# Optimization experiments

Hardware: AMD Instinct MI355X
Metric: run time of the kernel (lower is better)

## Reference

```python
import jax, jax.numpy as jnp
import numpy as np

B, L, D, H = 4, 2048, 2048, 16
HD = D // H
ROPE_BASE = 10000.0


def _rope_cos_sin(seq_len, dim):
    # torchtune-style: theta_i = base^{-2i/dim}, angles[t, i] = t * theta_i
    inv_freq = 1.0 / (ROPE_BASE ** (jnp.arange(0, dim, 2, dtype=jnp.float32) / dim))  # [dim/2]
    angles = jnp.arange(seq_len, dtype=jnp.float32)[:, None] * inv_freq[None, :]  # [L, dim/2]
    return jnp.cos(angles), jnp.sin(angles)


def _apply_rope(x, cos, sin):
    # x: [B, L, H, hd]; rotate interleaved pairs (x0, x1)
    x1 = x[..., 0::2]  # [B, L, H, hd/2]
    x2 = x[..., 1::2]
    c = cos[None, :, None, :]
    s = sin[None, :, None, :]
    o1 = x1 * c - x2 * s
    o2 = x2 * c + x1 * s
    return jnp.stack([o1, o2], axis=-1).reshape(x.shape)


def setup_inputs() -> dict:
    key = jax.random.key(0)
    k1, k2, k3 = jax.random.split(key, 3)
    x = jax.random.normal(k1, (B, L, D), dtype=jnp.float32)
    w_qkv = jax.random.normal(k2, (3 * D, D), dtype=jnp.float32) * (D ** -0.5)
    w_o = jax.random.normal(k3, (D, D), dtype=jnp.float32) * (D ** -0.5)
    return {"x": x, "w_qkv": w_qkv, "w_o": w_o}


def reference(x, w_qkv, w_o):
    qkv = jnp.einsum("bld,ed->ble", x, w_qkv)  # [B, L, 3D]
    q, k, v = jnp.split(qkv, 3, axis=-1)
    q = q.reshape(B, L, H, HD)
    k = k.reshape(B, L, H, HD)
    v = v.reshape(B, L, H, HD)
    cos, sin = _rope_cos_sin(L, HD)
    q = _apply_rope(q, cos, sin)
    k = _apply_rope(k, cos, sin)
    # [B, H, L, hd]
    q = q.transpose(0, 2, 1, 3)
    k = k.transpose(0, 2, 1, 3)
    v = v.transpose(0, 2, 1, 3)
    scores = jnp.einsum("bhqd,bhkd->bhqk", q, k) * (HD ** -0.5)
    causal = jnp.tril(jnp.ones((L, L), dtype=bool))
    scores = jnp.where(causal[None, None], scores, jnp.finfo(scores.dtype).min)
    attn = jax.nn.softmax(scores, axis=-1)
    y = jnp.einsum("bhqk,bhkd->bhqd", attn, v)
    y = y.transpose(0, 2, 1, 3).reshape(B, L, D)
    return jnp.einsum("bld,ed->ble", y, w_o)
```

## Files before the change

kernel.cpp:

```cpp
#include <hip/hip_runtime.h>

#define L_SEQ 2048
#define DMODEL 2048
#define NHEAD 16
#define HDIM 128
#define BATCH 4

typedef _Float16 f16x8 __attribute__((ext_vector_type(8)));
typedef _Float16 f16x4 __attribute__((ext_vector_type(4)));
typedef float f32x4 __attribute__((ext_vector_type(4)));

__device__ __forceinline__ void gload16(const void* g, void* l) {
  __builtin_amdgcn_global_load_lds((const __attribute__((address_space(1))) void*)g,
                                   (__attribute__((address_space(3))) void*)l, 16, 0, 0);
}

__global__ __launch_bounds__(256) void cvt_blocked(const float* __restrict__ in,
                                                   _Float16* __restrict__ out, int K) {
  const int kt = blockIdx.x, mb = blockIdx.y, KT = K >> 6;
  const int t = threadIdx.x, row = t >> 1, half = t & 1;
  const float* src = in + (size_t)(mb * 128 + row) * K + kt * 64 + half * 32;
  _Float16* tile = out + ((size_t)mb * KT + kt) * 8192;
  for (int j = 0; j < 4; ++j) {
    float4 a = *(const float4*)(src + j * 8);
    float4 b = *(const float4*)(src + j * 8 + 4);
    f16x8 o;
    o[0] = (_Float16)a.x; o[1] = (_Float16)a.y; o[2] = (_Float16)a.z; o[3] = (_Float16)a.w;
    o[4] = (_Float16)b.x; o[5] = (_Float16)b.y; o[6] = (_Float16)b.z; o[7] = (_Float16)b.w;
    int kb = half * 4 + j;
    *(f16x8*)(tile + (size_t)(kb * 128 + row) * 8) = o;
  }
}

template <typename OUT>
__global__ __launch_bounds__(256, 4) void gemm_bt(const _Float16* __restrict__ A,
                                                  const _Float16* __restrict__ Bt,
                                                  OUT* __restrict__ C,
                                                  int M, int N, int K) {
  __shared__ _Float16 As[128 * 64];
  __shared__ _Float16 Bs[128 * 64];
  const int KT = K >> 6;
  const int tid = threadIdx.x;
  const int wave = tid >> 6, lane = tid & 63, quad = lane >> 4, l15 = lane & 15;
  const int xcd = blockIdx.x & 7;
  const int lm = blockIdx.x >> 3;
  const int tm = xcd * 8 + (lm & 7);
  const int tn = lm >> 3;
  if (tm * 128 >= M || tn * 128 >= N) return;
  const int wm = (wave >> 1) * 64, wn = (wave & 1) * 64;
  const int id = wave * 4;
  f32x4 acc[4][4] = {};
  for (int kt = 0; kt < KT; ++kt) {
    const _Float16* tA = A + ((size_t)tm * KT + kt) * 8192;
    const _Float16* tB = Bt + ((size_t)tn * KT + kt) * 8192;
    __syncthreads();
    for (int j = 0; j < 4; ++j) {
      gload16(tA + (size_t)(id + j) * 512 + lane * 8, (char*)As + (id + j) * 1024);
      gload16(tB + (size_t)(id + j) * 512 + lane * 8, (char*)Bs + (id + j) * 1024);
    }
    __syncthreads();
    const f16x8* A8 = (const f16x8*)As;
    const f16x8* B8 = (const f16x8*)Bs;
    for (int kk = 0; kk < 2; ++kk) {
      int kb = kk * 4 + quad;
      f16x8 af[4], bf[4];
      for (int mi = 0; mi < 4; ++mi) af[mi] = A8[kb * 128 + wm + mi * 16 + l15];
      for (int ni = 0; ni < 4; ++ni) bf[ni] = B8[kb * 128 + wn + ni * 16 + l15];
      for (int mi = 0; mi < 4; ++mi)
        for (int ni = 0; ni < 4; ++ni)
          acc[mi][ni] = __builtin_amdgcn_mfma_f32_16x16x32_f16(af[mi], bf[ni], acc[mi][ni], 0, 0, 0);
    }
  }
  for (int mi = 0; mi < 4; ++mi)
    for (int ni = 0; ni < 4; ++ni) {
      int r = tm * 128 + wm + mi * 16 + quad * 4;
      int c = tn * 128 + wn + ni * 16 + l15;
      for (int reg = 0; reg < 4; ++reg)
        C[(size_t)(r + reg) * N + c] = (OUT)acc[mi][ni][reg];
    }
}

__global__ void rope_scatter(const _Float16* __restrict__ qkv,
                             _Float16* __restrict__ qt,
                             _Float16* __restrict__ kt) {
  int row = blockIdx.x;
  int pe = blockIdx.y * 256 + threadIdx.x;
  int e = pe * 2;
  float x1 = (float)qkv[(size_t)row * 6144 + e];
  float x2 = (float)qkv[(size_t)row * 6144 + e + 1];
  int which = e >> 11;
  int h = (e >> 7) & 15;
  int hd = e & 127;
  int b = row >> 11, l = row & 2047;
  int bh = b * 16 + h;
  int i = hd >> 1;
  float ang = (float)l * __expf((float)i * -0.14391156831212787f);
  float s, c;
  __sincosf(ang, &s, &c);
  float o1 = x1 * c - x2 * s;
  float o2 = x2 * c + x1 * s;
  _Float16* dst = (which == 0) ? qt : kt;
  size_t base = ((size_t)bh * 2048 + l) * 128 + hd;
  dst[base] = (_Float16)o1;
  dst[base + 1] = (_Float16)o2;
}

__global__ __launch_bounds__(256) void v_transpose(const _Float16* __restrict__ qkv,
                                                   _Float16* __restrict__ vt) {
  __shared__ _Float16 Ls[64 * 72];
  const int tid = threadIdx.x;
  const int l0 = blockIdx.x * 64;
  const int hd0 = blockIdx.y * 64;
  const int bh = blockIdx.z;
  const int b = bh >> 4, h = bh & 15;
  const size_t colbase = 4096 + h * 128 + hd0;
  for (int i = 0; i < 2; ++i) {
    int chunk = tid + i * 256;
    int r = chunk >> 3, c = chunk & 7;
    f16x8 v = *(const f16x8*)(qkv + (size_t)(b * 2048 + l0 + r) * 6144 + colbase + c * 8);
    *(f16x8*)(Ls + r * 72 + c * 8) = v;
  }
  __syncthreads();
  for (int i = 0; i < 2; ++i) {
    int chunk = tid + i * 256;
    int hr = chunk >> 3, c = chunk & 7;
    f16x8 o;
    for (int j = 0; j < 8; ++j) o[j] = Ls[(c * 8 + j) * 72 + hr];
    *(f16x8*)(vt + ((size_t)bh * 128 + hd0 + hr) * 2048 + l0 + c * 8) = o;
  }
}

__global__ __launch_bounds__(512, 4) void attn_fwd(const _Float16* __restrict__ qt,
                                                   const _Float16* __restrict__ kt,
                                                   const _Float16* __restrict__ vt,
                                                   _Float16* __restrict__ y) {
  __shared__ _Float16 Kl[64 * 128];
  __shared__ _Float16 Vl[64 * 128];
  __shared__ _Float16 Pl[8 * 16 * 64];
  const int a = blockIdx.y >> 2, bq = blockIdx.y & 3;
  const int qb = (a == 0) ? 15 - bq : (a == 1) ? 8 + bq : (a == 2) ? 4 + bq : 3 - bq;
  const int q0 = qb * 128;
  const int bh = blockIdx.x;
  const int tid = threadIdx.x;
  const int wave = tid >> 6, lane = tid & 63, quad = lane >> 4, l15 = lane & 15;
  const _Float16* Q = qt + (size_t)bh * L_SEQ * HDIM;
  const _Float16* Kg = kt + (size_t)bh * L_SEQ * HDIM;
  const _Float16* Vg = vt + (size_t)bh * HDIM * L_SEQ;

  const float scale = 0.08838834764831845f;
  f16x8 qf[4];
  {
    int qrow = q0 + wave * 16 + l15;
    const _Float16 hs = (_Float16)scale;
    for (int kk = 0; kk < 4; ++kk) {
      qf[kk] = *(const f16x8*)(Q + (size_t)qrow * 128 + kk * 32 + quad * 8);
      for (int j = 0; j < 8; ++j) qf[kk][j] *= hs;
    }
  }
  f32x4 o[8] = {};
  float mi[4] = {-1e30f, -1e30f, -1e30f, -1e30f};
  float li[4] = {0.f, 0.f, 0.f, 0.f};
  const int ntile = 2 * qb + 2;

  auto stageK = [&](int kv0) {
    for (int j = 0; j < 2; ++j) {
      int id = wave * 2 + j;
      gload16(Kg + (size_t)(kv0 + lane) * 128 + id * 8, (char*)Kl + id * 1024);
    }
  };
  auto stageV = [&](int kv0) {
    for (int j = 0; j < 2; ++j) {
      int id = wave * 2 + j;
      int kvb = id >> 1, h0 = (id & 1) * 64;
      gload16(Vg + (size_t)(h0 + lane) * L_SEQ + (kv0 + kvb * 8), (char*)Vl + (kvb * 128 + h0) * 16);
    }
  };

  stageK(0);
  stageV(0);

  for (int t = 0; t < ntile; ++t) {
    const int kv0 = t * 64;
    const bool more = (t + 1) < ntile;

    asm volatile("s_waitcnt vmcnt(2)" ::: "memory");
    __builtin_amdgcn_sched_barrier(0);
    __builtin_amdgcn_s_barrier();

    f32x4 s[4] = {};
    {
      const f16x8* K8 = (const f16x8*)Kl;
      __builtin_amdgcn_s_setprio(1);
      for (int kk = 0; kk < 4; ++kk) {
        int hb = kk * 4 + quad;
        for (int ni = 0; ni < 4; ++ni) {
          f16x8 bfr = K8[hb * 64 + ni * 16 + l15];
          s[ni] = __builtin_amdgcn_mfma_f32_16x16x32_f16(qf[kk], bfr, s[ni], 0, 0, 0);
        }
      }
      __builtin_amdgcn_s_setprio(0);
    }
    __builtin_amdgcn_sched_barrier(0);
    __builtin_amdgcn_s_barrier();
    __builtin_amdgcn_sched_barrier(0);
    if (more) stageK(kv0 + 64);

    float mx[4];
    if (t >= ntile - 2) {
      for (int reg = 0; reg < 4; ++reg) {
        int rowg = q0 + wave * 16 + quad * 4 + reg;
        float m = -1e30f;
        for (int ni = 0; ni < 4; ++ni) {
          float v = s[ni][reg];
          if ((kv0 + ni * 16 + l15) > rowg) v = -1e30f;
          s[ni][reg] = v;
          m = fmaxf(m, v);
        }
        mx[reg] = m;
      }
    } else {
      for (int reg = 0; reg < 4; ++reg)
        mx[reg] = fmaxf(fmaxf(s[0][reg], s[1][reg]), fmaxf(s[2][reg], s[3][reg]));
    }
    for (int off = 1; off < 16; off <<= 1)
      for (int reg = 0; reg < 4; ++reg)
        mx[reg] = fmaxf(mx[reg], __shfl_xor(mx[reg], off));
    float dm = fmaxf(fmaxf(mx[0] - mi[0], mx[1] - mi[1]),
                     fmaxf(mx[2] - mi[2], mx[3] - mi[3]));
    if (!__all(dm <= 8.0f)) {
      for (int reg = 0; reg < 4; ++reg) {
        float mn = fmaxf(mi[reg], mx[reg]);
        float al = __expf(mi[reg] - mn);
        mi[reg] = mn;
        li[reg] *= al;
        for (int ni = 0; ni < 8; ++ni) o[ni][reg] *= al;
      }
    }
    float rs[4] = {0.f, 0.f, 0.f, 0.f};
    _Float16* Pw = Pl + wave * (16 * 64);
    for (int ni = 0; ni < 4; ++ni) {
      int kv = ni * 16 + l15;
      int pbase = ((kv >> 3) * 16) * 8 + (kv & 7);
      for (int reg = 0; reg < 4; ++reg) {
        float p = __expf(s[ni][reg] - mi[reg]);
        rs[reg] += p;
        Pw[pbase + (quad * 4 + reg) * 8] = (_Float16)p;
      }
    }
    for (int off = 1; off < 16; off <<= 1)
      for (int reg = 0; reg < 4; ++reg)
        rs[reg] += __shfl_xor(rs[reg], off);
    for (int reg = 0; reg < 4; ++reg) li[reg] += rs[reg];

    if (more) {
      asm volatile("s_waitcnt vmcnt(2) lgkmcnt(0)" ::: "memory");
    } else {
      asm volatile("s_waitcnt vmcnt(0) lgkmcnt(0)" ::: "memory");
    }
    __builtin_amdgcn_sched_barrier(0);
    __builtin_amdgcn_s_barrier();

    {
      const f16x8* V8 = (const f16x8*)Vl;
      const f16x8* P8 = (const f16x8*)Pw;
      __builtin_amdgcn_s_setprio(1);
      for (int kk = 0; kk < 2; ++kk) {
        f16x8 pf = P8[(kk * 4 + quad) * 16 + l15];
        for (int ni = 0; ni < 8; ++ni) {
          f16x8 vf = V8[(kk * 4 + quad) * 128 + ni * 16 + l15];
          o[ni] = __builtin_amdgcn_mfma_f32_16x16x32_f16(pf, vf, o[ni], 0, 0, 0);
        }
      }
      __builtin_amdgcn_s_setprio(0);
    }
    __builtin_amdgcn_sched_barrier(0);
    __builtin_amdgcn_s_barrier();
    __builtin_amdgcn_sched_barrier(0);
    if (more) stageV(kv0 + 64);
  }
  int b = bh >> 4, h = bh & 15;
  for (int reg = 0; reg < 4; ++reg) {
    float inv = 1.f / li[reg];
    int gr = b * L_SEQ + q0 + wave * 16 + quad * 4 + reg;
    int mbt = gr >> 7, row = gr & 127;
    for (int ni = 0; ni < 8; ++ni) {
      int col = h * 128 + ni * 16 + l15;
      int cb = col >> 6, kb = (col >> 3) & 7, wi = col & 7;
      y[((size_t)mbt * 32 + cb) * 8192 + (size_t)(kb * 128 + row) * 8 + wi] =
          (_Float16)(o[ni][reg] * inv);
    }
  }
}

extern "C" void kernel_launch(void* const* d_in, const int* in_sizes, int n_in,
                              void* d_out, int out_size, void* d_ws, size_t ws_size,
                              hipStream_t stream) {
  const float* x = (const float*)d_in[0];
  const float* w_qkv = (const float*)d_in[1];
  const float* w_o = (const float*)d_in[2];
  float* out = (float*)d_out;

  char* ws = (char*)d_ws;
  _Float16* xb = (_Float16*)ws;    ws += (size_t)8192 * 2048 * 2;
  _Float16* wqkvb = (_Float16*)ws; ws += (size_t)6144 * 2048 * 2;
  _Float16* wob = (_Float16*)ws;   ws += (size_t)2048 * 2048 * 2;
  _Float16* qkv = (_Float16*)ws;   ws += (size_t)8192 * 6144 * 2;
  _Float16* qt = (_Float16*)ws;    ws += (size_t)64 * 2048 * 128 * 2;
  _Float16* kt = (_Float16*)ws;    ws += (size_t)64 * 2048 * 128 * 2;
  _Float16* vt = (_Float16*)ws;    ws += (size_t)64 * 2048 * 128 * 2;
  _Float16* y = qkv;

  cvt_blocked<<<dim3(32, 64), 256, 0, stream>>>(x, xb, 2048);
  cvt_blocked<<<dim3(32, 48), 256, 0, stream>>>(w_qkv, wqkvb, 2048);
  cvt_blocked<<<dim3(32, 16), 256, 0, stream>>>(w_o, wob, 2048);

  gemm_bt<_Float16><<<dim3(48 * 64), 256, 0, stream>>>(xb, wqkvb, qkv, 8192, 6144, 2048);
  rope_scatter<<<dim3(8192, 8), 256, 0, stream>>>(qkv, qt, kt);
  v_transpose<<<dim3(32, 2, 64), 256, 0, stream>>>(qkv, vt);
  attn_fwd<<<dim3(64, 16), 512, 0, stream>>>(qt, kt, vt, y);
  gemm_bt<float><<<dim3(16 * 64), 256, 0, stream>>>(y, wob, out, 8192, 2048, 2048);
}
```

Before: 643.0 us.

## Double-buffer GEMM LDS tiles to overlap global loads with MFMA compute

The GEMM kernel now keeps two LDS buffers for the A and B tiles and issues the global-to-LDS loads for the next K-tile before computing on the current one. It uses explicit vmcnt waits, s_barrier calls and setprio hints so memory latency overlaps with MFMA work instead of stalling on every iteration. LDS use doubles to 64KB per block, which can cut how many blocks fit on each CU below the launch_bounds target of 4.

After: 649.0 us. Within noise of the previous version (+0.9%).

```diff
diff --git a/kernel.cpp b/kernel.cpp
--- a/kernel.cpp
+++ b/kernel.cpp
@@ -37,8 +37,8 @@
                                                   const _Float16* __restrict__ Bt,
                                                   OUT* __restrict__ C,
                                                   int M, int N, int K) {
-  __shared__ _Float16 As[128 * 64];
-  __shared__ _Float16 Bs[128 * 64];
+  __shared__ _Float16 As[2][128 * 64];
+  __shared__ _Float16 Bs[2][128 * 64];
   const int KT = K >> 6;
   const int tid = threadIdx.x;
   const int wave = tid >> 6, lane = tid & 63, quad = lane >> 4, l15 = lane & 15;
@@ -49,18 +49,34 @@
   if (tm * 128 >= M || tn * 128 >= N) return;
   const int wm = (wave >> 1) * 64, wn = (wave & 1) * 64;
   const int id = wave * 4;
+  const _Float16* tA0 = A + (size_t)tm * KT * 8192;
+  const _Float16* tB0 = Bt + (size_t)tn * KT * 8192;
+
+  auto stage = [&](int kt, int buf) {
+    const _Float16* tA = tA0 + (size_t)kt * 8192;
+    const _Float16* tB = tB0 + (size_t)kt * 8192;
+    for (int j = 0; j < 4; ++j) {
+      gload16(tA + (size_t)(id + j) * 512 + lane * 8, (char*)As[buf] + (id + j) * 1024);
+      gload16(tB + (size_t)(id + j) * 512 + lane * 8, (char*)Bs[buf] + (id + j) * 1024);
+    }
+  };
+
   f32x4 acc[4][4] = {};
+  stage(0, 0);
+  int cur = 0;
   for (int kt = 0; kt < KT; ++kt) {
-    const _Float16* tA = A + ((size_t)tm * KT + kt) * 8192;
-    const _Float16* tB = Bt + ((size_t)tn * KT + kt) * 8192;
-    __syncthreads();
-    for (int j = 0; j < 4; ++j) {
-      gload16(tA + (size_t)(id + j) * 512 + lane * 8, (char*)As + (id + j) * 1024);
-      gload16(tB + (size_t)(id + j) * 512 + lane * 8, (char*)Bs + (id + j) * 1024);
-    }
-    __syncthreads();
-    const f16x8* A8 = (const f16x8*)As;
-    const f16x8* B8 = (const f16x8*)Bs;
+    const bool more = (kt + 1) < KT;
+    if (more) {
+      stage(kt + 1, cur ^ 1);
+      asm volatile("s_waitcnt vmcnt(8)" ::: "memory");
+    } else {
+      asm volatile("s_waitcnt vmcnt(0)" ::: "memory");
+    }
+    __builtin_amdgcn_sched_barrier(0);
+    __builtin_amdgcn_s_barrier();
+    const f16x8* A8 = (const f16x8*)As[cur];
+    const f16x8* B8 = (const f16x8*)Bs[cur];
+    __builtin_amdgcn_s_setprio(1);
     for (int kk = 0; kk < 2; ++kk) {
       int kb = kk * 4 + quad;
       f16x8 af[4], bf[4];
@@ -70,6 +86,11 @@
         for (int ni = 0; ni < 4; ++ni)
           acc[mi][ni] = __builtin_amdgcn_mfma_f32_16x16x32_f16(af[mi], bf[ni], acc[mi][ni], 0, 0, 0);
     }
+    __builtin_amdgcn_s_setprio(0);
+    asm volatile("s_waitcnt lgkmcnt(0)" ::: "memory");
+    __builtin_amdgcn_sched_barrier(0);
+    __builtin_amdgcn_s_barrier();
+    cur ^= 1;
   }
   for (int mi = 0; mi < 4; ++mi)
     for (int ni = 0; ni < 4; ++ni) {
```
